# Kernel optimization log

Hardware: AMD Instinct MI355X
Metric: run time of the kernel (lower is better)

Reference implementation:

```python
import jax, jax.numpy as jnp
import numpy as np

NEG_BIG = -9e15
ALPHA = 0.2  # LeakyReLU negative slope


def setup_inputs() -> dict:
    key = jax.random.key(0)
    k1, k2, k3, k4 = jax.random.split(key, 4)
    N, Fin, Fout = 8192, 256, 256
    input_ = jax.random.normal(k1, (N, Fin), dtype=jnp.float32)
    adj = jax.random.randint(k2, (N, N), 0, 2, dtype=jnp.int32)
    # xavier_uniform with gain=1.414
    limW = 1.414 * np.sqrt(6.0 / (Fin + Fout))
    W = jax.random.uniform(k3, (Fin, Fout), minval=-limW, maxval=limW, dtype=jnp.float32)
    lima = 1.414 * np.sqrt(6.0 / (2 * Fout + 1))
    a = jax.random.uniform(k4, (2 * Fout, 1), minval=-lima, maxval=lima, dtype=jnp.float32)
    return {"input_": input_, "adj": adj, "W": W, "a": a}


def reference(input_, adj, W, a):
    # h: [N, F]
    h = input_ @ W
    F = h.shape[1]
    # Decompose cat([h_i, h_j]) @ a into per-node projections summed by broadcast
    src = h @ a[:F, 0]   # [N]  contribution of row node i
    dst = h @ a[F:, 0]   # [N]  contribution of col node j
    e = jax.nn.leaky_relu(src[:, None] + dst[None, :], negative_slope=ALPHA)  # [N, N]
    e = jnp.where(adj > 0, e, NEG_BIG)
    attention = jax.nn.softmax(e, axis=1)
    h_prime = attention @ h  # [N, F]
    return jax.nn.relu(h_prime)  # concat=True
```

## Files before the change

### kernel.cpp

```cpp
#include <hip/hip_runtime.h>
#include <math.h>

#define NN 8192
#define FF 256
#define ALPHA 0.2f
#define SS 8
#define JSEG (NN / SS)
#define STEPS (JSEG / 32)
#define BI 128

typedef __bf16 bf16x8 __attribute__((ext_vector_type(8)));
typedef __bf16 bf16x4 __attribute__((ext_vector_type(4)));
typedef float  f32x4  __attribute__((ext_vector_type(4)));

__device__ __forceinline__ void dma16(const void* g, void* l) {
    __builtin_amdgcn_global_load_lds((const __attribute__((address_space(1))) void*)g,
                                     (__attribute__((address_space(3))) void*)l,
                                     16, 0, 0);
}

#define VMCNT0   asm volatile("s_waitcnt vmcnt(0)" ::: "memory")
#define LGKM0    asm volatile("s_waitcnt lgkmcnt(0)" ::: "memory")
#define BARRIER  asm volatile("s_barrier" ::: "memory")
#define FENCE    asm volatile("" ::: "memory")

__global__ __launch_bounds__(256) void k0_wt(const float* __restrict__ W,
                                             __bf16* __restrict__ WT) {
    __shared__ float ts[64][65];
    const int t = threadIdx.x;
    const int k0 = blockIdx.x * 64;
    const int n0 = blockIdx.y * 64;
    #pragma unroll
    for (int r = 0; r < 4; ++r) {
        int krow = r * 16 + (t >> 4);
        int nc4 = (t & 15) * 4;
        *(float4*)&ts[krow][nc4] = *(const float4*)&W[(size_t)(k0 + krow) * FF + n0 + nc4];
    }
    __syncthreads();
    const int nloc = t >> 2;
    const int kc = (t & 3) * 16;
    union { bf16x8 v[2]; __bf16 e[16]; } hi, lo;
    #pragma unroll
    for (int u = 0; u < 16; ++u) {
        float x = ts[kc + u][nloc];
        __bf16 h1 = (__bf16)x;
        hi.e[u] = h1;
        lo.e[u] = (__bf16)(x - (float)h1);
    }
    size_t base = (size_t)(n0 + nloc) * FF + k0 + kc;
    *(bf16x8*)&WT[base] = hi.v[0];
    *(bf16x8*)&WT[base + 8] = hi.v[1];
    size_t lbase = (size_t)FF * FF + base;
    *(bf16x8*)&WT[lbase] = lo.v[0];
    *(bf16x8*)&WT[lbase + 8] = lo.v[1];
}

__global__ __launch_bounds__(256) void k1_h(const float* __restrict__ X,
                                            const __bf16* __restrict__ WT,
                                            const float* __restrict__ a,
                                            __bf16* __restrict__ hT,
                                            float* __restrict__ src,
                                            float* __restrict__ dst) {
    __shared__ __bf16 ax[2][32][40];
    __shared__ float hs[32][264];
    __shared__ float red[2][4][32];
    const int t = threadIdx.x;
    const int i0 = blockIdx.x * 32;
    const int l = t & 63, wv = t >> 6, ln = l & 15, g = l >> 4;
    f32x4 acc[2][4];
    #pragma unroll
    for (int mt = 0; mt < 2; ++mt)
        #pragma unroll
        for (int nt = 0; nt < 4; ++nt)
            acc[mt][nt] = (f32x4){0.f, 0.f, 0.f, 0.f};

    for (int ks = 0; ks < 8; ++ks) {
        const int k0 = ks * 32;
        {
            int row = t >> 3, c4 = (t & 7) * 4;
            float4 xv = *(const float4*)&X[(size_t)(i0 + row) * FF + k0 + c4];
            bf16x4 hi4, lo4;
            float xs_[4] = {xv.x, xv.y, xv.z, xv.w};
            #pragma unroll
            for (int u = 0; u < 4; ++u) {
                __bf16 h1 = (__bf16)xs_[u];
                hi4[u] = h1;
                lo4[u] = (__bf16)(xs_[u] - (float)h1);
            }
            *(bf16x4*)&ax[0][row][c4] = hi4;
            *(bf16x4*)&ax[1][row][c4] = lo4;
        }
        __syncthreads();
        bf16x8 ah[2], al[2];
        ah[0] = *(bf16x8*)&ax[0][ln][g * 8];
        ah[1] = *(bf16x8*)&ax[0][16 + ln][g * 8];
        al[0] = *(bf16x8*)&ax[1][ln][g * 8];
        al[1] = *(bf16x8*)&ax[1][16 + ln][g * 8];
        #pragma unroll
        for (int nt = 0; nt < 4; ++nt) {
            const int n = wv * 64 + nt * 16 + ln;
            bf16x8 bh8 = *(const bf16x8*)&WT[(size_t)n * FF + k0 + g * 8];
            bf16x8 bl8 = *(const bf16x8*)&WT[(size_t)(FF + n) * FF + k0 + g * 8];
            #pragma unroll
            for (int mt = 0; mt < 2; ++mt) {
                acc[mt][nt] = __builtin_amdgcn_mfma_f32_16x16x32_bf16(ah[mt], bh8, acc[mt][nt], 0, 0, 0);
                acc[mt][nt] = __builtin_amdgcn_mfma_f32_16x16x32_bf16(ah[mt], bl8, acc[mt][nt], 0, 0, 0);
                acc[mt][nt] = __builtin_amdgcn_mfma_f32_16x16x32_bf16(al[mt], bh8, acc[mt][nt], 0, 0, 0);
            }
        }
        __syncthreads();
    }
    float an[4], ad[4];
    #pragma unroll
    for (int nt = 0; nt < 4; ++nt) {
        an[nt] = a[wv * 64 + nt * 16 + ln];
        ad[nt] = a[FF + wv * 64 + nt * 16 + ln];
    }
    float sp[2][4], dp[2][4];
    #pragma unroll
    for (int mt = 0; mt < 2; ++mt)
        #pragma unroll
        for (int rg = 0; rg < 4; ++rg) { sp[mt][rg] = 0.f; dp[mt][rg] = 0.f; }
    #pragma unroll
    for (int mt = 0; mt < 2; ++mt)
        #pragma unroll
        for (int nt = 0; nt < 4; ++nt)
            #pragma unroll
            for (int rg = 0; rg < 4; ++rg) {
                float v = acc[mt][nt][rg];
                hs[mt * 16 + g * 4 + rg][wv * 64 + nt * 16 + ln] = v;
                sp[mt][rg] += v * an[nt];
                dp[mt][rg] += v * ad[nt];
            }
    #pragma unroll
    for (int mk = 1; mk < 16; mk <<= 1)
        #pragma unroll
        for (int mt = 0; mt < 2; ++mt)
            #pragma unroll
            for (int rg = 0; rg < 4; ++rg) {
                sp[mt][rg] += __shfl_xor(sp[mt][rg], mk);
                dp[mt][rg] += __shfl_xor(dp[mt][rg], mk);
            }
    if (ln == 0) {
        #pragma unroll
        for (int mt = 0; mt < 2; ++mt)
            #pragma unroll
            for (int rg = 0; rg < 4; ++rg) {
                red[0][wv][mt * 16 + g * 4 + rg] = sp[mt][rg];
                red[1][wv][mt * 16 + g * 4 + rg] = dp[mt][rg];
            }
    }
    __syncthreads();
    if (t < 32) {
        src[i0 + t] = red[0][0][t] + red[0][1][t] + red[0][2][t] + red[0][3][t];
        dst[i0 + t] = red[1][0][t] + red[1][1][t] + red[1][2][t] + red[1][3][t];
    }
    {
        const int f = t;
        #pragma unroll
        for (int jc = 0; jc < 4; ++jc) {
            union { bf16x8 v; __bf16 e[8]; } hi;
            #pragma unroll
            for (int u = 0; u < 8; ++u) {
                float x = hs[jc * 8 + u][f];
                hi.e[u] = (__bf16)x;
            }
            *(bf16x8*)&hT[(size_t)f * NN + i0 + jc * 8] = hi.v;
        }
    }
}

__global__ __launch_bounds__(256) void k2a_pack(const int* __restrict__ adj,
                                                unsigned* __restrict__ bits) {
    const size_t total4 = (size_t)NN * NN / 4;
    const int l = threadIdx.x & 63;
    const int base = l & 56;
    size_t t = (size_t)blockIdx.x * 256 + threadIdx.x;
    const size_t stride = (size_t)gridDim.x * 256;
    for (; t < total4; t += stride) {
        int4 v = ((const int4*)adj)[t];
        unsigned nib = (unsigned)(v.x > 0) | ((unsigned)(v.y > 0) << 1)
                     | ((unsigned)(v.z > 0) << 2) | ((unsigned)(v.w > 0) << 3);
        unsigned w = 0;
        #pragma unroll
        for (int k = 0; k < 8; ++k)
            w |= (unsigned)__shfl((int)nib, base + k) << (4 * k);
        if ((l & 7) == 0)
            bits[t >> 3] = w;
    }
}

__global__ __launch_bounds__(256) void k2b_max(const float* __restrict__ dst,
                                               float* __restrict__ maxd) {
    __shared__ float red[256];
    float m = -1e30f;
    #pragma unroll
    for (int r = 0; r < NN / 1024; ++r) {
        float4 v = *(const float4*)&dst[(r * 256 + threadIdx.x) * 4];
        m = fmaxf(m, fmaxf(fmaxf(v.x, v.y), fmaxf(v.z, v.w)));
    }
    red[threadIdx.x] = m;
    __syncthreads();
    for (int s = 128; s > 0; s >>= 1) {
        if (threadIdx.x < s) red[threadIdx.x] = fmaxf(red[threadIdx.x], red[threadIdx.x + s]);
        __syncthreads();
    }
    if (threadIdx.x == 0) maxd[0] = red[0];
}

__global__ __launch_bounds__(512, 4) void k3_attn(const unsigned* __restrict__ bits,
                                                  const __bf16* __restrict__ hT,
                                                  const float* __restrict__ src,
                                                  const float* __restrict__ dst,
                                                  const float* __restrict__ maxd,
                                                  float* __restrict__ num,
                                                  float* __restrict__ den) {
    __shared__ __bf16 bh[2][1024 * 8];
    __shared__ float dsts[JSEG];
    const int t = threadIdx.x;
    const int l = t & 63, wv = t >> 6, ln = l & 15, g = l >> 4;
    const int it = blockIdx.x & 63;
    const int seg = blockIdx.x >> 6;
    const int i0 = it * BI;
    const int jbeg = seg * JSEG;
    const int row = i0 + wv * 16 + ln;
    const float maxdv = maxd[0];
    const float src_r = src[row];
    const float e0 = src_r + maxdv;
    const float m_r = e0 > 0.f ? e0 : ALPHA * e0;

    int ga[2], cb[2];
    #pragma unroll
    for (int r = 0; r < 2; ++r) {
        int cbase = r * 512 + wv * 64;
        int c = cbase + l;
        int f = c >> 2;
        int pc = c & 3;
        int jc = pc ^ ((f >> 1) & 3);
        ga[r] = f * NN + jc * 8;
        cb[r] = __builtin_amdgcn_readfirstlane(cbase);
    }
    const int rb = ln * 64 + ((g ^ ((ln >> 1) & 3)) * 16);
    const char* bh0 = (const char*)&bh[0][0] + rb;
    const char* bh1 = (const char*)&bh[1][0] + rb;

    const unsigned* grow = bits + (size_t)row * (NN / 32) + (jbeg >> 5);

    #pragma unroll
    for (int r = 0; r < 2; ++r)
        dma16(&hT[ga[r] + jbeg], &bh[0][cb[r] * 8]);
    FENCE;
    if (t < 256) *(float4*)&dsts[t * 4] = *(const float4*)&dst[jbeg + t * 4];
    uint2 wp = *(const uint2*)&grow[0];
    uint2 wpn = wp;
    __syncthreads();

    float den_reg = 0.f;
    f32x4 acc[16];
    #pragma unroll
    for (int nt = 0; nt < 16; ++nt) acc[nt] = (f32x4){0.f, 0.f, 0.f, 0.f};

#define K3_WCOMP(S_, MW_, AF_)                                                \
    {                                                                         \
        unsigned mb = ((MW_) >> (g * 8)) & 0xffu;                             \
        const float* dp_ = &dsts[(S_) * 32 + g * 8];                          \
        float4 dq0 = *(const float4*)dp_;                                     \
        float4 dq1 = *(const float4*)(dp_ + 4);                               \
        const float dv[8] = {dq0.x, dq0.y, dq0.z, dq0.w,                      \
                             dq1.x, dq1.y, dq1.z, dq1.w};                     \
        _Pragma("unroll")                                                     \
        for (int u = 0; u < 8; ++u) {                                         \
            float e = src_r + dv[u];                                          \
            e = e > 0.f ? e : ALPHA * e;                                      \
            float ex = __expf(e - m_r);                                       \
            float w = (mb & (1u << u)) ? ex : 0.f;                            \
            den_reg += w;                                                     \
            AF_.e[u] = (__bf16)w;                                             \
        }                                                                     \
    }

#define K3_MFMA(AF_, BP_)                                                     \
    {                                                                         \
        _Pragma("unroll")                                                     \
        for (int nt = 0; nt < 16; ++nt) {                                     \
            bf16x8 bfr = *(const bf16x8*)((BP_) + nt * 1024);                 \
            acc[nt] = __builtin_amdgcn_mfma_f32_16x16x32_bf16(                \
                AF_.v, bfr, acc[nt], 0, 0, 0);                                \
        }                                                                     \
    }

    for (int s = 0; s < STEPS; s += 2) {
        union { bf16x8 v; __bf16 e[8]; } afe;
        K3_WCOMP(s, wp.x, afe);
        FENCE; VMCNT0; LGKM0; BARRIER;
        #pragma unroll
        for (int r = 0; r < 2; ++r)
            dma16(&hT[ga[r] + jbeg + (s + 1) * 32], &bh[1][cb[r] * 8]);
        if (s + 2 < STEPS) wpn = *(const uint2*)&grow[s + 2];
        FENCE;
        K3_MFMA(afe, bh0);
        union { bf16x8 v; __bf16 e[8]; } afo;
        K3_WCOMP(s + 1, wp.y, afo);
        FENCE; VMCNT0; LGKM0; BARRIER;
        {
            int sn = (s + 2 < STEPS) ? s + 2 : 0;
            #pragma unroll
            for (int r = 0; r < 2; ++r)
                dma16(&hT[ga[r] + jbeg + sn * 32], &bh[0][cb[r] * 8]);
        }
        FENCE;
        K3_MFMA(afo, bh1);
        wp = wpn;
    }
    den_reg += __shfl_xor(den_reg, 16);
    den_reg += __shfl_xor(den_reg, 32);
    if (g == 0) den[(size_t)seg * NN + row] = den_reg;
    #pragma unroll
    for (int nt = 0; nt < 16; ++nt)
        #pragma unroll
        for (int rg = 0; rg < 4; ++rg)
            num[((size_t)seg * NN + i0 + wv * 16 + g * 4 + rg) * FF
                + nt * 16 + ln] = acc[nt][rg];
}

__global__ __launch_bounds__(256) void k4_out(const float* __restrict__ num,
                                              const float* __restrict__ den,
                                              float* __restrict__ out) {
    size_t f4 = (size_t)blockIdx.x * 256 + threadIdx.x;
    int i = (int)(f4 >> 6);
    int c4 = (int)(f4 & 63) << 2;
    float4 s = make_float4(0.f, 0.f, 0.f, 0.f);
    float d = 0.f;
    #pragma unroll
    for (int sg = 0; sg < SS; ++sg) {
        float4 v = *(const float4*)&num[((size_t)sg * NN + i) * FF + c4];
        s.x += v.x; s.y += v.y; s.z += v.z; s.w += v.w;
        d += den[(size_t)sg * NN + i];
    }
    float inv = 1.f / d;
    float4 o;
    o.x = fmaxf(s.x * inv, 0.f);
    o.y = fmaxf(s.y * inv, 0.f);
    o.z = fmaxf(s.z * inv, 0.f);
    o.w = fmaxf(s.w * inv, 0.f);
    *(float4*)&out[(size_t)i * FF + c4] = o;
}

extern "C" void kernel_launch(void* const* d_in, const int* in_sizes, int n_in,
                              void* d_out, int out_size, void* d_ws, size_t ws_size,
                              hipStream_t stream) {
    const float* X  = (const float*)d_in[0];
    const int*  adj = (const int*)d_in[1];
    const float* W  = (const float*)d_in[2];
    const float* a  = (const float*)d_in[3];
    float* out = (float*)d_out;
    char* ws = (char*)d_ws;

    const size_t off_hT   = 0;
    const size_t off_wt   = off_hT + (size_t)FF * NN * 2;
    const size_t off_src  = off_wt + (size_t)2 * FF * FF * 2;
    const size_t off_dst  = off_src + (size_t)NN * 4;
    const size_t off_maxd = off_dst + (size_t)NN * 4;
    const size_t off_num  = off_maxd + 256;
    const size_t off_den  = off_num + (size_t)SS * NN * FF * 4;
    const size_t off_bits = off_den + (size_t)SS * NN * 4;

    __bf16* hT_ws = (__bf16*)(ws + off_hT);
    __bf16* wt_ws = (__bf16*)(ws + off_wt);
    float* src_ws = (float*)(ws + off_src);
    float* dst_ws = (float*)(ws + off_dst);
    float* maxd   = (float*)(ws + off_maxd);
    float* num_ws = (float*)(ws + off_num);
    float* den_ws = (float*)(ws + off_den);
    unsigned* bits_ws = (unsigned*)(ws + off_bits);

    k2a_pack<<<2048, 256, 0, stream>>>(adj, bits_ws);
    k0_wt<<<dim3(FF / 64, FF / 64), 256, 0, stream>>>(W, wt_ws);
    k1_h<<<NN / 32, 256, 0, stream>>>(X, wt_ws, a, hT_ws, src_ws, dst_ws);
    k2b_max<<<1, 256, 0, stream>>>(dst_ws, maxd);
    k3_attn<<<(NN / BI) * SS, 512, 0, stream>>>(bits_ws, hT_ws, src_ws, dst_ws, maxd,
                                                num_ws, den_ws);
    k4_out<<<(NN * FF / 4) / 256, 256, 0, stream>>>(num_ws, den_ws, out);
}
```

Before: 446.4 us.

## Switch attention kernel to 32x32 MFMA with direct register B loads

Rewrites the main attention-aggregation kernel to use 32x32x16 bf16 MFMA tiles, with each wave owning 32 rows. The LDS double-buffered DMA staging of hT and its per-step barriers are removed. B fragments are loaded straight from global memory into registers with software double buffering, and block indexing is reordered so the eight segments of a row tile sit in adjacent blocks. This cuts LDS traffic and barrier sync, but each wave now reads hT from global/L2 on its own with no sharing through LDS, and register pressure goes up.

```diff
diff --git a/kernel.cpp b/kernel.cpp
--- a/kernel.cpp
+++ b/kernel.cpp
@@ -12,17 +12,7 @@
 typedef __bf16 bf16x8 __attribute__((ext_vector_type(8)));
 typedef __bf16 bf16x4 __attribute__((ext_vector_type(4)));
 typedef float  f32x4  __attribute__((ext_vector_type(4)));
-
-__device__ __forceinline__ void dma16(const void* g, void* l) {
-    __builtin_amdgcn_global_load_lds((const __attribute__((address_space(1))) void*)g,
-                                     (__attribute__((address_space(3))) void*)l,
-                                     16, 0, 0);
-}
-
-#define VMCNT0   asm volatile("s_waitcnt vmcnt(0)" ::: "memory")
-#define LGKM0    asm volatile("s_waitcnt lgkmcnt(0)" ::: "memory")
-#define BARRIER  asm volatile("s_barrier" ::: "memory")
-#define FENCE    asm volatile("" ::: "memory")
+typedef float  f32x16 __attribute__((ext_vector_type(16)));
 
 __global__ __launch_bounds__(256) void k0_wt(const float* __restrict__ W,
                                              __bf16* __restrict__ WT) {
@@ -208,62 +198,51 @@
     if (threadIdx.x == 0) maxd[0] = red[0];
 }
 
-__global__ __launch_bounds__(512, 4) void k3_attn(const unsigned* __restrict__ bits,
+__global__ __launch_bounds__(256, 2) void k3_attn(const unsigned* __restrict__ bits,
                                                   const __bf16* __restrict__ hT,
                                                   const float* __restrict__ src,
                                                   const float* __restrict__ dst,
                                                   const float* __restrict__ maxd,
                                                   float* __restrict__ num,
                                                   float* __restrict__ den) {
-    __shared__ __bf16 bh[2][1024 * 8];
     __shared__ float dsts[JSEG];
     const int t = threadIdx.x;
-    const int l = t & 63, wv = t >> 6, ln = l & 15, g = l >> 4;
-    const int it = blockIdx.x & 63;
-    const int seg = blockIdx.x >> 6;
+    const int l = t & 63, wv = t >> 6;
+    const int q = l & 31, hi = l >> 5;
+    const int seg = blockIdx.x & 7;
+    const int it = blockIdx.x >> 3;
     const int i0 = it * BI;
     const int jbeg = seg * JSEG;
-    const int row = i0 + wv * 16 + ln;
+    const int row = i0 + wv * 32 + q;
     const float maxdv = maxd[0];
     const float src_r = src[row];
     const float e0 = src_r + maxdv;
     const float m_r = e0 > 0.f ? e0 : ALPHA * e0;
 
-    int ga[2], cb[2];
-    #pragma unroll
-    for (int r = 0; r < 2; ++r) {
-        int cbase = r * 512 + wv * 64;
-        int c = cbase + l;
-        int f = c >> 2;
-        int pc = c & 3;
-        int jc = pc ^ ((f >> 1) & 3);
-        ga[r] = f * NN + jc * 8;
-        cb[r] = __builtin_amdgcn_readfirstlane(cbase);
-    }
-    const int rb = ln * 64 + ((g ^ ((ln >> 1) & 3)) * 16);
-    const char* bh0 = (const char*)&bh[0][0] + rb;
-    const char* bh1 = (const char*)&bh[1][0] + rb;
-
+    *(float4*)&dsts[t * 4] = *(const float4*)&dst[jbeg + t * 4];
+    __syncthreads();
+
+    const __bf16* bp = hT + (size_t)q * NN + 8 * hi;
     const unsigned* grow = bits + (size_t)row * (NN / 32) + (jbeg >> 5);
 
-    #pragma unroll
-    for (int r = 0; r < 2; ++r)
-        dma16(&hT[ga[r] + jbeg], &bh[0][cb[r] * 8]);
-    FENCE;
-    if (t < 256) *(float4*)&dsts[t * 4] = *(const float4*)&dst[jbeg + t * 4];
-    uint2 wp = *(const uint2*)&grow[0];
-    uint2 wpn = wp;
-    __syncthreads();
-
     float den_reg = 0.f;
-    f32x4 acc[16];
-    #pragma unroll
-    for (int nt = 0; nt < 16; ++nt) acc[nt] = (f32x4){0.f, 0.f, 0.f, 0.f};
-
-#define K3_WCOMP(S_, MW_, AF_)                                                \
+    f32x16 acc[8];
+    #pragma unroll
+    for (int ft = 0; ft < 8; ++ft)
+        #pragma unroll
+        for (int rg = 0; rg < 16; ++rg) acc[ft][rg] = 0.f;
+
+#define K3_LOADB(B_, J16_)                                                    \
     {                                                                         \
-        unsigned mb = ((MW_) >> (g * 8)) & 0xffu;                             \
-        const float* dp_ = &dsts[(S_) * 32 + g * 8];                          \
+        _Pragma("unroll")                                                     \
+        for (int ft = 0; ft < 8; ++ft)                                        \
+            B_[ft] = *(const bf16x8*)(bp + (size_t)ft * 32 * NN + (J16_));    \
+    }
+
+#define K3_WCOMP(S_, MW_, KOFF_, AF_)                                         \
+    {                                                                         \
+        unsigned mb = ((MW_) >> ((KOFF_) + 8 * hi)) & 0xffu;                  \
+        const float* dp_ = &dsts[(S_) * 32 + (KOFF_) + 8 * hi];               \
         float4 dq0 = *(const float4*)dp_;                                     \
         float4 dq1 = *(const float4*)(dp_ + 4);                               \
         const float dv[8] = {dq0.x, dq0.y, dq0.z, dq0.w,                      \
@@ -279,48 +258,43 @@
         }                                                                     \
     }
 
-#define K3_MFMA(AF_, BP_)                                                     \
+#define K3_MFMA(AF_, B_)                                                      \
     {                                                                         \
         _Pragma("unroll")                                                     \
-        for (int nt = 0; nt < 16; ++nt) {                                     \
-            bf16x8 bfr = *(const bf16x8*)((BP_) + nt * 1024);                 \
-            acc[nt] = __builtin_amdgcn_mfma_f32_16x16x32_bf16(                \
-                AF_.v, bfr, acc[nt], 0, 0, 0);                                \
-        }                                                                     \
-    }
-
-    for (int s = 0; s < STEPS; s += 2) {
+        for (int ft = 0; ft < 8; ++ft)                                        \
+            acc[ft] = __builtin_amdgcn_mfma_f32_32x32x16_bf16(                \
+                AF_.v, B_[ft], acc[ft], 0, 0, 0);                             \
+    }
+
+    bf16x8 BE[8], BO[8];
+    K3_LOADB(BE, jbeg);
+    unsigned mw = grow[0];
+
+    for (int s = 0; s < STEPS; ++s) {
+        const int j16 = jbeg + s * 32;
+        unsigned mwn = grow[(s + 1 < STEPS) ? s + 1 : 0];
+        K3_LOADB(BO, j16 + 16);
         union { bf16x8 v; __bf16 e[8]; } afe;
-        K3_WCOMP(s, wp.x, afe);
-        FENCE; VMCNT0; LGKM0; BARRIER;
-        #pragma unroll
-        for (int r = 0; r < 2; ++r)
-            dma16(&hT[ga[r] + jbeg + (s + 1) * 32], &bh[1][cb[r] * 8]);
-        if (s + 2 < STEPS) wpn = *(const uint2*)&grow[s + 2];
-        FENCE;
-        K3_MFMA(afe, bh0);
+        K3_WCOMP(s, mw, 0, afe);
+        K3_MFMA(afe, BE);
+        {
+            const int jn = (s + 1 < STEPS) ? j16 + 32 : jbeg;
+            K3_LOADB(BE, jn);
+        }
         union { bf16x8 v; __bf16 e[8]; } afo;
-        K3_WCOMP(s + 1, wp.y, afo);
-        FENCE; VMCNT0; LGKM0; BARRIER;
-        {
-            int sn = (s + 2 < STEPS) ? s + 2 : 0;
-            #pragma unroll
-            for (int r = 0; r < 2; ++r)
-                dma16(&hT[ga[r] + jbeg + sn * 32], &bh[0][cb[r] * 8]);
-        }
-        FENCE;
-        K3_MFMA(afo, bh1);
-        wp = wpn;
-    }
-    den_reg += __shfl_xor(den_reg, 16);
+        K3_WCOMP(s, mw, 16, afo);
+        K3_MFMA(afo, BO);
+        mw = mwn;
+    }
     den_reg += __shfl_xor(den_reg, 32);
-    if (g == 0) den[(size_t)seg * NN + row] = den_reg;
-    #pragma unroll
-    for (int nt = 0; nt < 16; ++nt)
-        #pragma unroll
-        for (int rg = 0; rg < 4; ++rg)
-            num[((size_t)seg * NN + i0 + wv * 16 + g * 4 + rg) * FF
-                + nt * 16 + ln] = acc[nt][rg];
+    if (hi == 0) den[(size_t)seg * NN + row] = den_reg;
+    #pragma unroll
+    for (int ft = 0; ft < 8; ++ft)
+        #pragma unroll
+        for (int rg = 0; rg < 16; ++rg) {
+            int m = (rg & 3) + 8 * (rg >> 2) + 4 * hi;
+            num[((size_t)seg * NN + i0 + wv * 32 + m) * FF + ft * 32 + q] = acc[ft][rg];
+        }
 }
 
 __global__ __launch_bounds__(256) void k4_out(const float* __restrict__ num,
@@ -378,7 +352,7 @@
     k0_wt<<<dim3(FF / 64, FF / 64), 256, 0, stream>>>(W, wt_ws);
     k1_h<<<NN / 32, 256, 0, stream>>>(X, wt_ws, a, hT_ws, src_ws, dst_ws);
     k2b_max<<<1, 256, 0, stream>>>(dst_ws, maxd);
-    k3_attn<<<(NN / BI) * SS, 512, 0, stream>>>(bits_ws, hT_ws, src_ws, dst_ws, maxd,
+    k3_attn<<<(NN / BI) * SS, 256, 0, stream>>>(bits_ws, hT_ws, src_ws, dst_ws, maxd,
                                                 num_ws, den_ws);
     k4_out<<<(NN * FF / 4) / 256, 256, 0, stream>>>(num_ws, den_ws, out);
 }
```

Measured after the change: 525.4 us. 17.7% more time.
